# Kernel optimization log

Measured on AMD Instinct MI355X. Metric: run time of the kernel, lower is better.

The kernel has to match this reference:

```python
import jax, jax.numpy as jnp
import numpy as np

B, C, H, W = 64, 3, 256, 256
P = 8            # patch size (neib_shape = (8, 8))
NC = 512         # num_cells
F = C * P * P    # 192 flattened patch features


def setup_inputs() -> dict:
    key = jax.random.key(0)
    k0, k1, k2 = jax.random.split(key, 3)
    s = 1.0 / np.sqrt(NC)  # torch nn.LSTM init scale
    return {
        "x": jax.random.normal(k0, (B, C, H, W), jnp.float32),
        "W_ih": jax.random.uniform(k1, (4 * NC, F + NC), jnp.float32, -s, s),
        "W_hh": jax.random.uniform(k2, (4 * NC, NC), jnp.float32, -s, s),
        "b_ih": jnp.zeros((4 * NC,), jnp.float32),
        "b_hh": jnp.zeros((4 * NC,), jnp.float32),
    }


def reference(x, W_ih, W_hh, b_ih, b_hh):
    Bn, Cn, Hi, Wi = x.shape
    sy, sx = Hi // P, Wi // P
    T = sy * sx
    # Row-major patch sequence, flattening (C, p, p) per patch -> (T, B, F)
    xp = x.reshape(Bn, Cn, sy, P, sx, P)
    xp = xp.transpose(2, 4, 0, 1, 3, 5).reshape(T, Bn, Cn * P * P)

    bias = b_ih + b_hh

    def step(carry, xt):
        h, c, buf = carry                       # buf: (sx, B, NC) ring of last sx outputs
        prev2 = buf[0]                          # output from sx steps ago (patch above)
        inp = jnp.concatenate([xt, prev2], axis=-1)   # (B, F+NC)
        gates = inp @ W_ih.T + h @ W_hh.T + bias      # (B, 4*NC)
        i_, f_, g_, o_ = jnp.split(gates, 4, axis=-1) # torch gate order i,f,g,o
        c = jax.nn.sigmoid(f_) * c + jax.nn.sigmoid(i_) * jnp.tanh(g_)
        h = jax.nn.sigmoid(o_) * jnp.tanh(c)
        buf = jnp.concatenate([buf[1:], h[None]], axis=0)
        return (h, c, buf), h

    h0 = jnp.zeros((Bn, NC), x.dtype)
    c0 = jnp.zeros((Bn, NC), x.dtype)
    buf0 = jnp.zeros((sx, Bn, NC), x.dtype)   # queue yields zeros for first sx steps
    _, outs = jax.lax.scan(step, (h0, c0, buf0), xp)  # outs: (T, B, NC)

    # to_image: cat -> permute (B,T,NC) -> reshape (B, NC, sy, sx) (row-major, as torch)
    return outs.transpose(1, 0, 2).reshape(Bn, NC, sy, sx)
```

## Files before the change

kernel.cpp:

```cpp
#include <hip/hip_runtime.h>
#include <hip/hip_fp16.h>


typedef __attribute__((ext_vector_type(8))) _Float16 half8;
typedef __attribute__((ext_vector_type(4))) float f32x4;
typedef unsigned long long u64;

#define T_ 1024

#define LDS_W    77824
#define LDS_PSM  33792
#define LDS_ALL  (LDS_W + LDS_PSM + 512)

extern __shared__ char smem[];

__global__ __launch_bounds__(512, 1) void lstm_persist(
    const float* __restrict__ x, const float* __restrict__ Wih,
    const float* __restrict__ Whh, const float* __restrict__ bih,
    const float* __restrict__ bhh, float* __restrict__ out,
    u64* ring)
{
    _Float16* Wsm = (_Float16*)smem;
    float*    Psm = (float*)(smem + LDS_W);
    float*    cst = (float*)(smem + LDS_W + LDS_PSM);

    const int tid = threadIdx.x;
    const int l   = tid & 63, wv = tid >> 6;
    const int l15 = l & 15,  l4 = l >> 4;
    const int bid = blockIdx.x;
    const int g   = bid >> 6;
    const int w   = bid & 63;

    for (int p = wv; p < 76; p += 8) {
        const int c = p >> 1, nb = p & 1;
        const int rj = (l15 & 3) * 512 + w * 8 + nb * 4 + (l15 >> 2);
        const int k  = c * 32 + l4 * 8;
        const float* src = (c < 22) ? (Wih + (size_t)rj * 704 + k)
                                    : (Whh + (size_t)rj * 512 + (k - 704));
        float4 v0 = ((const float4*)src)[0];
        float4 v1 = ((const float4*)src)[1];
        half8 hb;
        hb[0]=(_Float16)v0.x; hb[1]=(_Float16)v0.y; hb[2]=(_Float16)v0.z; hb[3]=(_Float16)v0.w;
        hb[4]=(_Float16)v1.x; hb[5]=(_Float16)v1.y; hb[6]=(_Float16)v1.z; hb[7]=(_Float16)v1.w;
        *(half8*)(Wsm + (size_t)((c * 2 + nb) * 64 + l) * 8) = hb;
    }
    if (tid < 128) cst[tid] = 0.f;

    const int pb = tid >> 3, pc = tid & 7;
    const int gc = w * 8 + pc;
    const float bI = bih[gc]        + bhh[gc];
    const float bF = bih[512 + gc]  + bhh[512 + gc];
    const float bG = bih[1024 + gc] + bhh[1024 + gc];
    const float bO = bih[1536 + gc] + bhh[1536 + gc];
    __syncthreads();

    const int coff = (wv + 2) & 7;
    const int c32a = 6 + coff,  c32b = 14 + coff;
    const int c1a  = 22 + coff, c1b  = 30 + coff;
    const int gb   = g * 16 + l15;

    auto wfrag = [&](int c, int nb) -> half8 {
        return *(const half8*)(Wsm + (size_t)((c * 2 + nb) * 64 + l) * 8);
    };
    auto loadfrag = [&](int slot, int cc, unsigned par_) -> half8 {
        const size_t idx = ((size_t)(slot * 4 + g)) * 2048 + (size_t)cc * 128 + 2 * l;
        const u64 M  = 0x0001000100010001ULL;
        const u64 ex = par_ ? M : 0ULL;
        u64 v0 = __hip_atomic_load(ring + idx,     __ATOMIC_RELAXED, __HIP_MEMORY_SCOPE_AGENT);
        u64 v1 = __hip_atomic_load(ring + idx + 1, __ATOMIC_RELAXED, __HIP_MEMORY_SCOPE_AGENT);
        bool ok = ((v0 & M) == ex) && ((v1 & M) == ex);
        while (!__all(ok)) {
            __builtin_amdgcn_s_sleep(1);
            if (!ok) {
                v0 = __hip_atomic_load(ring + idx,     __ATOMIC_RELAXED, __HIP_MEMORY_SCOPE_AGENT);
                v1 = __hip_atomic_load(ring + idx + 1, __ATOMIC_RELAXED, __HIP_MEMORY_SCOPE_AGENT);
                ok = ((v0 & M) == ex) && ((v1 & M) == ex);
            }
        }
        union { u64 u[2]; half8 h; } cc_;
        cc_.u[0] = v0; cc_.u[1] = v1;
        return cc_.h;
    };

    float4 xa0, xa1;
    half8  h32a, h32b;
    if (wv < 6) {
        const int k0 = wv * 32 + l4 * 8;
        const float* xs = x + ((size_t)(gb * 3 + (k0 >> 6)) * 256 + ((k0 >> 3) & 7)) * 256;
        xa0 = ((const float4*)xs)[0];
        xa1 = ((const float4*)xs)[1];
    }

    for (int t = 0; t < T_; ++t) {
        const int par = t & 1;
        f32x4 acc0 = {0.f,0.f,0.f,0.f}, acc1 = {0.f,0.f,0.f,0.f};

        if (wv < 6) {
            half8 a;
            a[0]=(_Float16)xa0.x; a[1]=(_Float16)xa0.y; a[2]=(_Float16)xa0.z; a[3]=(_Float16)xa0.w;
            a[4]=(_Float16)xa1.x; a[5]=(_Float16)xa1.y; a[6]=(_Float16)xa1.z; a[7]=(_Float16)xa1.w;
            acc0 = __builtin_amdgcn_mfma_f32_16x16x32_f16(a, wfrag(wv,0), acc0, 0,0,0);
            acc1 = __builtin_amdgcn_mfma_f32_16x16x32_f16(a, wfrag(wv,1), acc1, 0,0,0);
        }
        if (t >= 32) {
            acc0 = __builtin_amdgcn_mfma_f32_16x16x32_f16(h32a, wfrag(c32a,0), acc0, 0,0,0);
            acc1 = __builtin_amdgcn_mfma_f32_16x16x32_f16(h32a, wfrag(c32a,1), acc1, 0,0,0);
            acc0 = __builtin_amdgcn_mfma_f32_16x16x32_f16(h32b, wfrag(c32b,0), acc0, 0,0,0);
            acc1 = __builtin_amdgcn_mfma_f32_16x16x32_f16(h32b, wfrag(c32b,1), acc1, 0,0,0);
        }
        if (t > 0) {
            const int sP = (t - 1) & 63;
            const unsigned p1 = ((t - 1) >> 6) & 1;
            half8 ha = loadfrag(sP, c1a - 22, p1);
            acc0 = __builtin_amdgcn_mfma_f32_16x16x32_f16(ha, wfrag(c1a,0), acc0, 0,0,0);
            acc1 = __builtin_amdgcn_mfma_f32_16x16x32_f16(ha, wfrag(c1a,1), acc1, 0,0,0);
            half8 hb = loadfrag(sP, c1b - 22, p1);
            acc0 = __builtin_amdgcn_mfma_f32_16x16x32_f16(hb, wfrag(c1b,0), acc0, 0,0,0);
            acc1 = __builtin_amdgcn_mfma_f32_16x16x32_f16(hb, wfrag(c1b,1), acc1, 0,0,0);
        }

        {
            float* Pw = Psm + (size_t)((par * 8 + wv) * 16) * 33;
#pragma unroll
            for (int r = 0; r < 4; ++r) {
                Pw[(l4 * 4 + r) * 33 + l15]      = acc0[r];
                Pw[(l4 * 4 + r) * 33 + 16 + l15] = acc1[r];
            }
        }
        __syncthreads();

        if (tid < 128) {
            float gi = bI, gf = bF, gg = bG, go = bO;
#pragma unroll
            for (int q = 0; q < 8; ++q) {
                const float* Pq = Psm + ((size_t)((par * 8 + q) * 16 + pb)) * 33 + pc * 4;
                gi += Pq[0]; gf += Pq[1]; gg += Pq[2]; go += Pq[3];
            }
            const float cprev = cst[tid];
            const float si = 1.f / (1.f + __expf(-gi));
            const float sf = 1.f / (1.f + __expf(-gf));
            const float so = 1.f / (1.f + __expf(-go));
            const float tg = 2.f / (1.f + __expf(-2.f * gg)) - 1.f;
            const float cn = sf * cprev + si * tg;
            const float th = 2.f / (1.f + __expf(-2.f * cn)) - 1.f;
            const float hn = so * th;
            cst[tid] = cn;

            union { _Float16 f; unsigned short s; } cv; cv.f = (_Float16)hn;
            unsigned hb16 = ((unsigned)cv.s & ~1u) | (unsigned)((t >> 6) & 1);
            unsigned other = (unsigned)__shfl_xor((int)hb16, 1);
            unsigned pairv = (pc & 1) ? ((other & 0xffffu) | (hb16 << 16))
                                      : ((hb16 & 0xffffu) | (other << 16));
            unsigned hi = (unsigned)__shfl_xor((int)pairv, 2);
            if ((pc & 3) == 0) {
                u64 val = (u64)pairv | ((u64)hi << 32);
                const size_t idx = ((size_t)((t & 63) * 4 + g)) * 2048
                                 + (size_t)w * 32 + (size_t)pb * 2 + (pc >> 2);
                __hip_atomic_store(ring + idx, val, __ATOMIC_RELAXED,
                                   __HIP_MEMORY_SCOPE_AGENT);
            }
            out[(size_t)(g * 16 + pb) * (T_ * 512) + (size_t)t * 512 + gc] = hn;
        }

        const int tn = t + 1;
        if (tn < T_) {
            if (wv < 6) {
                const int yn = tn >> 5, xcn = tn & 31;
                const int k0 = wv * 32 + l4 * 8;
                const float* xs = x + ((size_t)(gb * 3 + (k0 >> 6)) * 256
                                       + yn * 8 + ((k0 >> 3) & 7)) * 256 + xcn * 8;
                xa0 = ((const float4*)xs)[0];
                xa1 = ((const float4*)xs)[1];
            }
            if (tn >= 32) {
                const int sO = (tn - 32) & 63;
                const unsigned p32 = ((tn - 32) >> 6) & 1;
                h32a = loadfrag(sO, c32a - 6, p32);
                h32b = loadfrag(sO, c32b - 6, p32);
            }
        }
    }
}

extern "C" void kernel_launch(void* const* d_in, const int* in_sizes, int n_in,
                              void* d_out, int out_size, void* d_ws, size_t ws_size,
                              hipStream_t stream) {
    const float* x   = (const float*)d_in[0];
    const float* Wih = (const float*)d_in[1];
    const float* Whh = (const float*)d_in[2];
    const float* bih = (const float*)d_in[3];
    const float* bhh = (const float*)d_in[4];
    float* out = (float*)d_out;

    u64* ring = (u64*)d_ws;

    hipMemsetAsync(ring, 0x01, 64ull * 4 * 2048 * 8, stream);

    (void)hipFuncSetAttribute((const void*)lstm_persist,
                              hipFuncAttributeMaxDynamicSharedMemorySize, LDS_ALL);

    hipLaunchKernelGGL(lstm_persist, dim3(256), dim3(512), LDS_ALL, stream,
                       x, Wih, Whh, bih, bhh, out, ring);
}
```

Baseline: 2.441 ms.

## Interleave two batch groups per block to overlap recurrent latency, halving grid

Each block now handles two batch groups (A and B) alternately within each timestep, using 128 blocks instead of 256. Group B's matmul work and ring loads can hide the wait on group A's cross-block handoff, and the t-32 ring values are now prefetched without spinning, with validity checked only when they are used. The cost is twice the serial work per block, an extra barrier per step, and fewer CUs in use, so the overlap has to outweigh the doubled per-block compute.

Result: slower. 4.231 ms (+73.3%).

```diff
diff --git a/kernel.cpp b/kernel.cpp
--- a/kernel.cpp
+++ b/kernel.cpp
@@ -10,9 +10,11 @@
 
 #define LDS_W    77824
 #define LDS_PSM  33792
-#define LDS_ALL  (LDS_W + LDS_PSM + 512)
+#define LDS_ALL  (LDS_W + LDS_PSM + 1024)
 
 extern __shared__ char smem[];
+
+union U2H { u64 u[2]; half8 h; };
 
 __global__ __launch_bounds__(512, 1) void lstm_persist(
     const float* __restrict__ x, const float* __restrict__ Wih,
@@ -28,8 +30,9 @@
     const int l   = tid & 63, wv = tid >> 6;
     const int l15 = l & 15,  l4 = l >> 4;
     const int bid = blockIdx.x;
-    const int g   = bid >> 6;
+    const int st  = bid >> 6;
     const int w   = bid & 63;
+    const int gA  = st * 2, gB = st * 2 + 1;
 
     for (int p = wv; p < 76; p += 8) {
         const int c = p >> 1, nb = p & 1;
@@ -44,141 +47,182 @@
         hb[4]=(_Float16)v1.x; hb[5]=(_Float16)v1.y; hb[6]=(_Float16)v1.z; hb[7]=(_Float16)v1.w;
         *(half8*)(Wsm + (size_t)((c * 2 + nb) * 64 + l) * 8) = hb;
     }
-    if (tid < 128) cst[tid] = 0.f;
-
-    const int pb = tid >> 3, pc = tid & 7;
-    const int gc = w * 8 + pc;
-    const float bI = bih[gc]        + bhh[gc];
-    const float bF = bih[512 + gc]  + bhh[512 + gc];
-    const float bG = bih[1024 + gc] + bhh[1024 + gc];
-    const float bO = bih[1536 + gc] + bhh[1536 + gc];
+    if (tid < 256) cst[tid] = 0.f;
+
+    const int pcb = tid & 7;
+    const int gcb = w * 8 + pcb;
+    const float bI = bih[gcb]        + bhh[gcb];
+    const float bF = bih[512 + gcb]  + bhh[512 + gcb];
+    const float bG = bih[1024 + gcb] + bhh[1024 + gcb];
+    const float bO = bih[1536 + gcb] + bhh[1536 + gcb];
     __syncthreads();
 
     const int coff = (wv + 2) & 7;
     const int c32a = 6 + coff,  c32b = 14 + coff;
     const int c1a  = 22 + coff, c1b  = 30 + coff;
-    const int gb   = g * 16 + l15;
+    const int gbA  = gA * 16 + l15, gbB = gB * 16 + l15;
 
     auto wfrag = [&](int c, int nb) -> half8 {
         return *(const half8*)(Wsm + (size_t)((c * 2 + nb) * 64 + l) * 8);
     };
-    auto loadfrag = [&](int slot, int cc, unsigned par_) -> half8 {
-        const size_t idx = ((size_t)(slot * 4 + g)) * 2048 + (size_t)cc * 128 + 2 * l;
-        const u64 M  = 0x0001000100010001ULL;
-        const u64 ex = par_ ? M : 0ULL;
-        u64 v0 = __hip_atomic_load(ring + idx,     __ATOMIC_RELAXED, __HIP_MEMORY_SCOPE_AGENT);
-        u64 v1 = __hip_atomic_load(ring + idx + 1, __ATOMIC_RELAXED, __HIP_MEMORY_SCOPE_AGENT);
-        bool ok = ((v0 & M) == ex) && ((v1 & M) == ex);
+    auto rld = [&](size_t i) -> u64 {
+        return __hip_atomic_load(ring + i, __ATOMIC_RELAXED, __HIP_MEMORY_SCOPE_AGENT);
+    };
+    auto ridx = [&](int slot, int g_, int cc) -> size_t {
+        return ((size_t)(slot * 4 + g_)) * 2048 + (size_t)cc * 128 + 2 * l;
+    };
+    const u64 TM = 0x0001000100010001ULL;
+
+    auto loadfrag = [&](int slot, int g_, int cc, unsigned par_) -> half8 {
+        const size_t idx = ridx(slot, g_, cc);
+        const u64 ex = par_ ? TM : 0ULL;
+        u64 v0 = rld(idx), v1 = rld(idx + 1);
+        bool ok = ((v0 & TM) == ex) && ((v1 & TM) == ex);
         while (!__all(ok)) {
             __builtin_amdgcn_s_sleep(1);
             if (!ok) {
-                v0 = __hip_atomic_load(ring + idx,     __ATOMIC_RELAXED, __HIP_MEMORY_SCOPE_AGENT);
-                v1 = __hip_atomic_load(ring + idx + 1, __ATOMIC_RELAXED, __HIP_MEMORY_SCOPE_AGENT);
-                ok = ((v0 & M) == ex) && ((v1 & M) == ex);
+                v0 = rld(idx); v1 = rld(idx + 1);
+                ok = ((v0 & TM) == ex) && ((v1 & TM) == ex);
             }
         }
-        union { u64 u[2]; half8 h; } cc_;
-        cc_.u[0] = v0; cc_.u[1] = v1;
+        U2H cc_; cc_.u[0] = v0; cc_.u[1] = v1;
         return cc_.h;
     };
 
-    float4 xa0, xa1;
-    half8  h32a, h32b;
-    if (wv < 6) {
+    auto xload = [&](int gb_, int t_, float4& r0, float4& r1) {
+        const int yn = t_ >> 5, xcn = t_ & 31;
         const int k0 = wv * 32 + l4 * 8;
-        const float* xs = x + ((size_t)(gb * 3 + (k0 >> 6)) * 256 + ((k0 >> 3) & 7)) * 256;
-        xa0 = ((const float4*)xs)[0];
-        xa1 = ((const float4*)xs)[1];
-    }
+        const float* xs = x + ((size_t)(gb_ * 3 + (k0 >> 6)) * 256
+                               + yn * 8 + ((k0 >> 3) & 7)) * 256 + xcn * 8;
+        r0 = ((const float4*)xs)[0];
+        r1 = ((const float4*)xs)[1];
+    };
+    auto xmfma = [&](float4 v0, float4 v1, f32x4& a0, f32x4& a1) {
+        half8 a;
+        a[0]=(_Float16)v0.x; a[1]=(_Float16)v0.y; a[2]=(_Float16)v0.z; a[3]=(_Float16)v0.w;
+        a[4]=(_Float16)v1.x; a[5]=(_Float16)v1.y; a[6]=(_Float16)v1.z; a[7]=(_Float16)v1.w;
+        a0 = __builtin_amdgcn_mfma_f32_16x16x32_f16(a, wfrag(wv,0), a0, 0,0,0);
+        a1 = __builtin_amdgcn_mfma_f32_16x16x32_f16(a, wfrag(wv,1), a1, 0,0,0);
+    };
+    auto h32part = [&](int t, int g_, u64& a0_, u64& a1_, u64& b0_, u64& b1_,
+                       f32x4& A0, f32x4& A1) {
+        const u64 ex = (((t - 32) >> 6) & 1) ? TM : 0ULL;
+        bool ok = ((a0_ & TM) == ex) && ((a1_ & TM) == ex) &&
+                  ((b0_ & TM) == ex) && ((b1_ & TM) == ex);
+        if (!__all(ok)) {
+            const size_t ia = ridx((t - 32) & 63, g_, c32a - 6);
+            const size_t ib = ridx((t - 32) & 63, g_, c32b - 6);
+            do {
+                __builtin_amdgcn_s_sleep(1);
+                if (!ok) {
+                    a0_ = rld(ia); a1_ = rld(ia + 1);
+                    b0_ = rld(ib); b1_ = rld(ib + 1);
+                    ok = ((a0_ & TM) == ex) && ((a1_ & TM) == ex) &&
+                         ((b0_ & TM) == ex) && ((b1_ & TM) == ex);
+                }
+            } while (!__all(ok));
+        }
+        U2H ca, cb;
+        ca.u[0] = a0_; ca.u[1] = a1_; cb.u[0] = b0_; cb.u[1] = b1_;
+        A0 = __builtin_amdgcn_mfma_f32_16x16x32_f16(ca.h, wfrag(c32a,0), A0, 0,0,0);
+        A1 = __builtin_amdgcn_mfma_f32_16x16x32_f16(ca.h, wfrag(c32a,1), A1, 0,0,0);
+        A0 = __builtin_amdgcn_mfma_f32_16x16x32_f16(cb.h, wfrag(c32b,0), A0, 0,0,0);
+        A1 = __builtin_amdgcn_mfma_f32_16x16x32_f16(cb.h, wfrag(c32b,1), A1, 0,0,0);
+    };
+    auto h1part = [&](int t, int g_, f32x4& A0, f32x4& A1) {
+        const int sP = (t - 1) & 63;
+        const unsigned p1 = ((t - 1) >> 6) & 1;
+        half8 ha = loadfrag(sP, g_, c1a - 22, p1);
+        A0 = __builtin_amdgcn_mfma_f32_16x16x32_f16(ha, wfrag(c1a,0), A0, 0,0,0);
+        A1 = __builtin_amdgcn_mfma_f32_16x16x32_f16(ha, wfrag(c1a,1), A1, 0,0,0);
+        half8 hb = loadfrag(sP, g_, c1b - 22, p1);
+        A0 = __builtin_amdgcn_mfma_f32_16x16x32_f16(hb, wfrag(c1b,0), A0, 0,0,0);
+        A1 = __builtin_amdgcn_mfma_f32_16x16x32_f16(hb, wfrag(c1b,1), A1, 0,0,0);
+    };
+    auto psmwrite = [&](int sub, f32x4 A0, f32x4 A1) {
+        float* Pw = Psm + (size_t)((sub * 8 + wv) * 16) * 33;
+#pragma unroll
+        for (int r = 0; r < 4; ++r) {
+            Pw[(l4 * 4 + r) * 33 + l15]      = A0[r];
+            Pw[(l4 * 4 + r) * 33 + 16 + l15] = A1[r];
+        }
+    };
+    auto pointwise = [&](int t, int g_, int sub, int tl) {
+        float gi = bI, gf = bF, gg = bG, go = bO;
+        const int pb_ = tl >> 3, pc_ = tl & 7;
+#pragma unroll
+        for (int q = 0; q < 8; ++q) {
+            const float* Pq = Psm + ((size_t)((sub * 8 + q) * 16 + pb_)) * 33 + pc_ * 4;
+            gi += Pq[0]; gf += Pq[1]; gg += Pq[2]; go += Pq[3];
+        }
+        const float cprev = cst[tid];
+        const float si = 1.f / (1.f + __expf(-gi));
+        const float sf = 1.f / (1.f + __expf(-gf));
+        const float so = 1.f / (1.f + __expf(-go));
+        const float tg = 2.f / (1.f + __expf(-2.f * gg)) - 1.f;
+        const float cn = sf * cprev + si * tg;
+        const float th = 2.f / (1.f + __expf(-2.f * cn)) - 1.f;
+        const float hn = so * th;
+        cst[tid] = cn;
+
+        union { _Float16 f; unsigned short s; } cv; cv.f = (_Float16)hn;
+        unsigned hb16 = ((unsigned)cv.s & ~1u) | (unsigned)((t >> 6) & 1);
+        unsigned other = (unsigned)__shfl_xor((int)hb16, 1);
+        unsigned pairv = (pc_ & 1) ? ((other & 0xffffu) | (hb16 << 16))
+                                   : ((hb16 & 0xffffu) | (other << 16));
+        unsigned hi = (unsigned)__shfl_xor((int)pairv, 2);
+        if ((pc_ & 3) == 0) {
+            u64 val = (u64)pairv | ((u64)hi << 32);
+            const size_t idx = ((size_t)((t & 63) * 4 + g_)) * 2048
+                             + (size_t)w * 32 + (size_t)pb_ * 2 + (pc_ >> 2);
+            __hip_atomic_store(ring + idx, val, __ATOMIC_RELAXED,
+                               __HIP_MEMORY_SCOPE_AGENT);
+        }
+        out[(size_t)(g_ * 16 + pb_) * (T_ * 512) + (size_t)t * 512 + w * 8 + pc_] = hn;
+    };
+
+    float4 xaA0, xaA1, xaB0, xaB1;
+    u64 hAa0=0,hAa1=0,hAb0=0,hAb1=0;
+    u64 hBa0=0,hBa1=0,hBb0=0,hBb1=0;
+
+    if (wv < 6) { xload(gbA, 0, xaA0, xaA1); xload(gbB, 0, xaB0, xaB1); }
 
     for (int t = 0; t < T_; ++t) {
-        const int par = t & 1;
+        const int tn = t + 1;
+
         f32x4 acc0 = {0.f,0.f,0.f,0.f}, acc1 = {0.f,0.f,0.f,0.f};
-
-        if (wv < 6) {
-            half8 a;
-            a[0]=(_Float16)xa0.x; a[1]=(_Float16)xa0.y; a[2]=(_Float16)xa0.z; a[3]=(_Float16)xa0.w;
-            a[4]=(_Float16)xa1.x; a[5]=(_Float16)xa1.y; a[6]=(_Float16)xa1.z; a[7]=(_Float16)xa1.w;
-            acc0 = __builtin_amdgcn_mfma_f32_16x16x32_f16(a, wfrag(wv,0), acc0, 0,0,0);
-            acc1 = __builtin_amdgcn_mfma_f32_16x16x32_f16(a, wfrag(wv,1), acc1, 0,0,0);
-        }
-        if (t >= 32) {
-            acc0 = __builtin_amdgcn_mfma_f32_16x16x32_f16(h32a, wfrag(c32a,0), acc0, 0,0,0);
-            acc1 = __builtin_amdgcn_mfma_f32_16x16x32_f16(h32a, wfrag(c32a,1), acc1, 0,0,0);
-            acc0 = __builtin_amdgcn_mfma_f32_16x16x32_f16(h32b, wfrag(c32b,0), acc0, 0,0,0);
-            acc1 = __builtin_amdgcn_mfma_f32_16x16x32_f16(h32b, wfrag(c32b,1), acc1, 0,0,0);
-        }
-        if (t > 0) {
-            const int sP = (t - 1) & 63;
-            const unsigned p1 = ((t - 1) >> 6) & 1;
-            half8 ha = loadfrag(sP, c1a - 22, p1);
-            acc0 = __builtin_amdgcn_mfma_f32_16x16x32_f16(ha, wfrag(c1a,0), acc0, 0,0,0);
-            acc1 = __builtin_amdgcn_mfma_f32_16x16x32_f16(ha, wfrag(c1a,1), acc1, 0,0,0);
-            half8 hb = loadfrag(sP, c1b - 22, p1);
-            acc0 = __builtin_amdgcn_mfma_f32_16x16x32_f16(hb, wfrag(c1b,0), acc0, 0,0,0);
-            acc1 = __builtin_amdgcn_mfma_f32_16x16x32_f16(hb, wfrag(c1b,1), acc1, 0,0,0);
-        }
-
-        {
-            float* Pw = Psm + (size_t)((par * 8 + wv) * 16) * 33;
-#pragma unroll
-            for (int r = 0; r < 4; ++r) {
-                Pw[(l4 * 4 + r) * 33 + l15]      = acc0[r];
-                Pw[(l4 * 4 + r) * 33 + 16 + l15] = acc1[r];
+        if (wv < 6) xmfma(xaA0, xaA1, acc0, acc1);
+        if (t >= 32) h32part(t, gA, hAa0, hAa1, hAb0, hAb1, acc0, acc1);
+        if (t > 0)  h1part(t, gA, acc0, acc1);
+        if (tn < T_) {
+            if (wv < 6) xload(gbA, tn, xaA0, xaA1);
+            if (tn >= 32) {
+                const size_t ia = ridx((tn - 32) & 63, gA, c32a - 6);
+                const size_t ib = ridx((tn - 32) & 63, gA, c32b - 6);
+                hAa0 = rld(ia); hAa1 = rld(ia + 1);
+                hAb0 = rld(ib); hAb1 = rld(ib + 1);
             }
         }
+        psmwrite(0, acc0, acc1);
         __syncthreads();
-
-        if (tid < 128) {
-            float gi = bI, gf = bF, gg = bG, go = bO;
-#pragma unroll
-            for (int q = 0; q < 8; ++q) {
-                const float* Pq = Psm + ((size_t)((par * 8 + q) * 16 + pb)) * 33 + pc * 4;
-                gi += Pq[0]; gf += Pq[1]; gg += Pq[2]; go += Pq[3];
+        if (tid < 128) pointwise(t, gA, 0, tid);
+
+        acc0 = (f32x4){0.f,0.f,0.f,0.f}; acc1 = (f32x4){0.f,0.f,0.f,0.f};
+        if (wv < 6) xmfma(xaB0, xaB1, acc0, acc1);
+        if (t >= 32) h32part(t, gB, hBa0, hBa1, hBb0, hBb1, acc0, acc1);
+        if (t > 0)  h1part(t, gB, acc0, acc1);
+        if (tn < T_) {
+            if (wv < 6) xload(gbB, tn, xaB0, xaB1);
+            if (tn >= 32) {
+                const size_t ia = ridx((tn - 32) & 63, gB, c32a - 6);
+                const size_t ib = ridx((tn - 32) & 63, gB, c32b - 6);
+                hBa0 = rld(ia); hBa1 = rld(ia + 1);
+                hBb0 = rld(ib); hBb1 = rld(ib + 1);
             }
-            const float cprev = cst[tid];
-            const float si = 1.f / (1.f + __expf(-gi));
-            const float sf = 1.f / (1.f + __expf(-gf));
-            const float so = 1.f / (1.f + __expf(-go));
-            const float tg = 2.f / (1.f + __expf(-2.f * gg)) - 1.f;
-            const float cn = sf * cprev + si * tg;
-            const float th = 2.f / (1.f + __expf(-2.f * cn)) - 1.f;
-            const float hn = so * th;
-            cst[tid] = cn;
-
-            union { _Float16 f; unsigned short s; } cv; cv.f = (_Float16)hn;
-            unsigned hb16 = ((unsigned)cv.s & ~1u) | (unsigned)((t >> 6) & 1);
-            unsigned other = (unsigned)__shfl_xor((int)hb16, 1);
-            unsigned pairv = (pc & 1) ? ((other & 0xffffu) | (hb16 << 16))
-                                      : ((hb16 & 0xffffu) | (other << 16));
-            unsigned hi = (unsigned)__shfl_xor((int)pairv, 2);
-            if ((pc & 3) == 0) {
-                u64 val = (u64)pairv | ((u64)hi << 32);
-                const size_t idx = ((size_t)((t & 63) * 4 + g)) * 2048
-                                 + (size_t)w * 32 + (size_t)pb * 2 + (pc >> 2);
-                __hip_atomic_store(ring + idx, val, __ATOMIC_RELAXED,
-                                   __HIP_MEMORY_SCOPE_AGENT);
-            }
-            out[(size_t)(g * 16 + pb) * (T_ * 512) + (size_t)t * 512 + gc] = hn;
-        }
-
-        const int tn = t + 1;
-        if (tn < T_) {
-            if (wv < 6) {
-                const int yn = tn >> 5, xcn = tn & 31;
-                const int k0 = wv * 32 + l4 * 8;
-                const float* xs = x + ((size_t)(gb * 3 + (k0 >> 6)) * 256
-                                       + yn * 8 + ((k0 >> 3) & 7)) * 256 + xcn * 8;
-                xa0 = ((const float4*)xs)[0];
-                xa1 = ((const float4*)xs)[1];
-            }
-            if (tn >= 32) {
-                const int sO = (tn - 32) & 63;
-                const unsigned p32 = ((tn - 32) >> 6) & 1;
-                h32a = loadfrag(sO, c32a - 6, p32);
-                h32b = loadfrag(sO, c32b - 6, p32);
-            }
-        }
+        }
+        psmwrite(1, acc0, acc1);
+        __syncthreads();
+        if (tid >= 128 && tid < 256) pointwise(t, gB, 1, tid - 128);
     }
 }
 
@@ -199,6 +243,6 @@
     (void)hipFuncSetAttribute((const void*)lstm_persist,
                               hipFuncAttributeMaxDynamicSharedMemorySize, LDS_ALL);
 
-    hipLaunchKernelGGL(lstm_persist, dim3(256), dim3(512), LDS_ALL, stream,
+    hipLaunchKernelGGL(lstm_persist, dim3(128), dim3(512), LDS_ALL, stream,
                        x, Wih, Whh, bih, bhh, out, ring);
 }
```
